# Optimization experiments

Measured on AMD Instinct MI355X. Metric: run time of the kernel, lower is better.

Reference implementation:

```python
import jax, jax.numpy as jnp
import numpy as np

T, N, E, D = 4, 50000, 800000, 256
VOCAB = 64000


def _gcn_layer(x, row, col, w, W, b, n):
    # PyG GCNConv: add self-loops (weight 1), symmetric normalization on
    # weighted in-degree (target/col), h = x @ W, scatter-add, then + bias.
    loops = jnp.arange(n, dtype=row.dtype)
    row2 = jnp.concatenate([row, loops])
    col2 = jnp.concatenate([col, loops])
    w2 = jnp.concatenate([w, jnp.ones((n,), x.dtype)])
    deg = jax.ops.segment_sum(w2, col2, num_segments=n)
    dinv = jnp.where(deg > 0, jax.lax.rsqrt(deg), 0.0)
    norm = dinv[row2] * w2 * dinv[col2]              # [E+N]
    h = x @ W                                        # [N, D]
    out = jax.ops.segment_sum(norm[:, None] * h[row2], col2, num_segments=n)
    return out + b


def _encode_timestep(ids, row, col, w, emb, W1, b1, W2, b2, W3, b3):
    x = emb[ids]                                     # [N, D] embedding lookup
    x = _gcn_layer(x, row, col, w, W1, b1, ids.shape[0])
    x = _gcn_layer(x, row, col, w, W2, b2, ids.shape[0])
    x = _gcn_layer(x, row, col, w, W3, b3, ids.shape[0])
    return x


def setup_inputs() -> dict:
    key = jax.random.key(0)
    ks = jax.random.split(key, 8)
    scale = 1.0 / np.sqrt(D)
    return {
        "node_features": jax.random.randint(ks[0], (T, N), 0, VOCAB, dtype=jnp.int32),
        "edge_index": jax.random.randint(ks[1], (T, 2, E), 0, N, dtype=jnp.int32),
        "edge_weight": jax.random.uniform(ks[2], (T, E), dtype=jnp.float32),
        "emb": jax.random.normal(ks[3], (VOCAB, D), dtype=jnp.float32),
        "W1": jax.random.normal(ks[4], (D, D), dtype=jnp.float32) * scale,
        "b1": jnp.zeros((D,), jnp.float32),
        "W2": jax.random.normal(ks[5], (D, D), dtype=jnp.float32) * scale,
        "b2": jnp.zeros((D,), jnp.float32),
        "W3": jax.random.normal(ks[6], (D, D), dtype=jnp.float32) * scale,
        "b3": jnp.zeros((D,), jnp.float32),
    }


def reference(node_features, edge_index, edge_weight, emb, W1, b1, W2, b2, W3, b3):
    outs = []
    for t in range(node_features.shape[0]):  # fixed small timestep count
        outs.append(_encode_timestep(node_features[t], edge_index[t, 0],
                                     edge_index[t, 1], edge_weight[t],
                                     emb, W1, b1, W2, b2, W3, b3))
    return jnp.concatenate(outs, axis=0)  # [T*N, D]
```

## Files before the change

kernel.cpp:

```cpp
#include <hip/hip_runtime.h>

#define T_STEPS 4
#define NN 50000
#define EE 800000
#define DD 256
#define VOCAB 64000
#define NB ((NN + 255) / 256)

typedef __attribute__((ext_vector_type(8))) short short8;
typedef __attribute__((ext_vector_type(4))) float floatx4;

__device__ __forceinline__ unsigned short f2bf(float f) {
    unsigned u = __float_as_uint(f);
    return (unsigned short)((u + 0x7FFFu + ((u >> 16) & 1u)) >> 16);
}
__device__ __forceinline__ float bf2f(unsigned short s) {
    return __uint_as_float(((unsigned)s) << 16);
}

__device__ __forceinline__ void async16(const unsigned short* g, unsigned short* l) {
    __builtin_amdgcn_global_load_lds(
        (const __attribute__((address_space(1))) void*)g,
        (__attribute__((address_space(3))) void*)l, 16, 0, 0);
}

__global__ __launch_bounds__(256) void init_deg_cnt(float* __restrict__ deg,
                                                    int* __restrict__ cnt, int n) {
    int i = blockIdx.x * 256 + threadIdx.x;
    if (i < n) { deg[i] = 1.0f; cnt[i] = 0; }
}

__global__ __launch_bounds__(256) void edge_deg_cnt(const int* __restrict__ col,
                                                    const float* __restrict__ w,
                                                    float* __restrict__ deg,
                                                    int* __restrict__ cnt, int e) {
    int i = blockIdx.x * 256 + threadIdx.x;
    if (i < e) {
        int c = col[i];
        atomicAdd(&deg[c], w[i]);
        atomicAdd(&cnt[c], 1);
    }
}

__global__ __launch_bounds__(256) void dinv_bsums(const float* __restrict__ deg,
                                                  float* __restrict__ dinv,
                                                  float* __restrict__ s1,
                                                  const int* __restrict__ cnt,
                                                  int* __restrict__ bsum, int n) {
    int i = blockIdx.x * 256 + threadIdx.x;
    if (i < n) {
        float d = deg[i];
        float r = d > 0.0f ? rsqrtf(d) : 0.0f;
        dinv[i] = r;
        s1[i] = r * r;
    }
    __shared__ int sm[256];
    sm[threadIdx.x] = (i < n) ? cnt[i] : 0;
    __syncthreads();
    for (int s = 128; s > 0; s >>= 1) {
        if ((int)threadIdx.x < s) sm[threadIdx.x] += sm[threadIdx.x + s];
        __syncthreads();
    }
    if (threadIdx.x == 0) bsum[blockIdx.x] = sm[0];
}

__global__ __launch_bounds__(256) void scan_bsum(const int* __restrict__ bsum,
                                                 int* __restrict__ boff, int nb) {
    __shared__ int sm[256];
    int v = ((int)threadIdx.x < nb) ? bsum[threadIdx.x] : 0;
    sm[threadIdx.x] = v;
    __syncthreads();
    for (int o = 1; o < 256; o <<= 1) {
        int t = (threadIdx.x >= (unsigned)o) ? sm[threadIdx.x - o] : 0;
        __syncthreads();
        sm[threadIdx.x] += t;
        __syncthreads();
    }
    if ((int)threadIdx.x < nb) boff[threadIdx.x] = sm[threadIdx.x] - v;
}

__global__ __launch_bounds__(256) void scan_final(const int* __restrict__ cnt,
                                                  const int* __restrict__ boff,
                                                  int* __restrict__ colptr,
                                                  int* __restrict__ next, int n, int e) {
    __shared__ int sm[256];
    int i = blockIdx.x * 256 + threadIdx.x;
    int v = (i < n) ? cnt[i] : 0;
    sm[threadIdx.x] = v;
    __syncthreads();
    for (int o = 1; o < 256; o <<= 1) {
        int t = (threadIdx.x >= (unsigned)o) ? sm[threadIdx.x - o] : 0;
        __syncthreads();
        sm[threadIdx.x] += t;
        __syncthreads();
    }
    int excl = sm[threadIdx.x] - v + boff[blockIdx.x];
    if (i < n) { colptr[i] = excl; next[i] = excl; }
    if (i == 0) colptr[n] = e;
}

__global__ __launch_bounds__(256) void fill_csr(const int* __restrict__ row,
                                                const int* __restrict__ col,
                                                const float* __restrict__ w,
                                                const float* __restrict__ dinv,
                                                int* __restrict__ next,
                                                int2* __restrict__ edges,
                                                float* __restrict__ s1, int e) {
    int i = blockIdx.x * 256 + threadIdx.x;
    if (i < e) {
        int r = row[i], c = col[i];
        float nm = dinv[r] * w[i] * dinv[c];
        int p = atomicAdd(&next[c], 1);
        edges[p] = make_int2(r, __float_as_int(nm));
        atomicAdd(&s1[c], nm);
    }
}

__global__ __launch_bounds__(256) void matmul256(const float* __restrict__ A,
                                                 const float* __restrict__ B,
                                                 float* __restrict__ C) {
    __shared__ float arow[256];
    int i = blockIdx.x, j = threadIdx.x;
    arow[j] = A[i * 256 + j];
    __syncthreads();
    float acc = 0.f;
#pragma unroll 8
    for (int k = 0; k < 256; ++k) acc += arow[k] * B[k * 256 + j];
    C[i * 256 + j] = acc;
}

__global__ __launch_bounds__(256) void matvec256(const float* __restrict__ x,
                                                 const float* __restrict__ W,
                                                 float* __restrict__ y) {
    __shared__ float xs[256];
    int j = threadIdx.x;
    xs[j] = x[j];
    __syncthreads();
    float acc = 0.f;
#pragma unroll 8
    for (int k = 0; k < 256; ++k) acc += xs[k] * W[k * 256 + j];
    y[j] = acc;
}

__global__ __launch_bounds__(256) void convert_wc(const float* __restrict__ Wc,
                                                  unsigned short* __restrict__ wt) {
    int n = blockIdx.x;
    int k = threadIdx.x;
    wt[n * 256 + k] = f2bf(Wc[k * 256 + n]);
}

__global__ __launch_bounds__(256) void convert_emb(const float* __restrict__ emb,
                                                   unsigned short* __restrict__ ebf,
                                                   int total4) {
    int t = blockIdx.x * 256 + threadIdx.x;
    if (t < total4) {
        float4 v = ((const float4*)emb)[t];
        ushort4 o;
        o.x = f2bf(v.x); o.y = f2bf(v.y); o.z = f2bf(v.z); o.w = f2bf(v.w);
        ((ushort4*)ebf)[t] = o;
    }
}

__global__ __launch_bounds__(256) void mfma_gemm(const int* __restrict__ ids,
                                                 const unsigned short* __restrict__ ebf,
                                                 const unsigned short* __restrict__ wt,
                                                 unsigned short* __restrict__ h2,
                                                 int M) {
    __shared__ __align__(16) unsigned short As[128 * 32];
    __shared__ __align__(16) unsigned short Bs[256 * 32];

    int tid = threadIdx.x;
    int lane = tid & 63;
    int wave = tid >> 6;
    int row0 = blockIdx.x * 128;
    int wm = (wave & 1) * 64;
    int wn = (wave >> 1) * 128;
    int quad = lane >> 4;
    int cl = lane & 15;

    int uA0 = tid, uA1 = 256 + tid;
    int cA0 = uA0 >> 7, mA0 = uA0 & 127;
    int cA1 = uA1 >> 7;
    int gr = row0 + mA0; if (gr >= M) gr = M - 1;
    int id0 = ids[gr];
    const unsigned short* srcA0 = ebf + (size_t)id0 * 256 + cA0 * 8;
    const unsigned short* srcA1 = ebf + (size_t)id0 * 256 + cA1 * 8;
    unsigned short* dstA0 = As + uA0 * 8;
    unsigned short* dstA1 = As + uA1 * 8;

    const unsigned short* srcB = wt + (size_t)tid * 256;
    unsigned short* dstBbase = Bs + tid * 8;

    floatx4 acc[4][8] = {};

    for (int k0 = 0; k0 < 256; k0 += 32) {
        if (k0) __syncthreads();
        async16(srcA0 + k0, dstA0);
        async16(srcA1 + k0, dstA1);
#pragma unroll
        for (int s5 = 0; s5 < 4; ++s5)
            async16(srcB + s5 * 8 + k0, dstBbase + s5 * 2048);
        __syncthreads();

        short8 af[4], bfr[8];
#pragma unroll
        for (int i = 0; i < 4; ++i)
            af[i] = *(const short8*)&As[(quad * 128 + wm + i * 16 + cl) * 8];
#pragma unroll
        for (int j = 0; j < 8; ++j)
            bfr[j] = *(const short8*)&Bs[(quad * 256 + wn + j * 16 + cl) * 8];
#pragma unroll
        for (int i = 0; i < 4; ++i)
#pragma unroll
            for (int j = 0; j < 8; ++j)
                acc[i][j] = __builtin_amdgcn_mfma_f32_16x16x32_bf16(
                    af[i], bfr[j], acc[i][j], 0, 0, 0);
    }

#pragma unroll
    for (int i = 0; i < 4; ++i) {
#pragma unroll
        for (int r = 0; r < 4; ++r) {
            int gr2 = row0 + wm + i * 16 + quad * 4 + r;
            if (gr2 < M) {
                size_t base = (size_t)gr2 * 256 + wn + cl;
#pragma unroll
                for (int j = 0; j < 8; ++j)
                    h2[base + j * 16] = f2bf(acc[i][j][r]);
            }
        }
    }
}

__global__ __launch_bounds__(256) void agg_kernel(const unsigned short* __restrict__ h2,
                                                  const int* __restrict__ colptr,
                                                  const int2* __restrict__ edges,
                                                  const float* __restrict__ dinv,
                                                  const float* __restrict__ s1,
                                                  float* __restrict__ s2_out,
                                                  const float* __restrict__ s2,
                                                  const float* __restrict__ v1,
                                                  const float* __restrict__ v2,
                                                  const float* __restrict__ b3,
                                                  float* __restrict__ dstf,
                                                  unsigned short* __restrict__ dstb,
                                                  int n) {
    int wave = threadIdx.x >> 6;
    int lane = threadIdx.x & 63;
    int h = lane >> 5;
    int s = lane & 31;
    int c = blockIdx.x * 4 + wave;
    if (c >= n) return;
    int p0 = colptr[c];
    int p1 = colptr[c + 1];
    float di = dinv[c];
    float self = di * di;
    bool do_s2 = (s2_out != nullptr);

    float accA[8] = {}, accB[8] = {};
    float ssA = 0.f, ssB = 0.f;

    if (h == 0) {
        short8 v = *(const short8*)(h2 + (size_t)c * 256 + s * 8);
#pragma unroll
        for (int k = 0; k < 8; ++k) accA[k] += self * bf2f((unsigned short)v[k]);
    }

    int j = p0 + h;
    for (; j + 2 < p1; j += 4) {
        int2 e0 = edges[j];
        int2 e1 = edges[j + 2];
        float w0 = __int_as_float(e0.y);
        float w1 = __int_as_float(e1.y);
        short8 va = *(const short8*)(h2 + (size_t)e0.x * 256 + s * 8);
        short8 vb = *(const short8*)(h2 + (size_t)e1.x * 256 + s * 8);
        if (do_s2) { ssA += w0 * s1[e0.x]; ssB += w1 * s1[e1.x]; }
#pragma unroll
        for (int k = 0; k < 8; ++k) {
            accA[k] += w0 * bf2f((unsigned short)va[k]);
            accB[k] += w1 * bf2f((unsigned short)vb[k]);
        }
    }
    if (j < p1) {
        int2 e0 = edges[j];
        float w0 = __int_as_float(e0.y);
        short8 va = *(const short8*)(h2 + (size_t)e0.x * 256 + s * 8);
        if (do_s2) ssA += w0 * s1[e0.x];
#pragma unroll
        for (int k = 0; k < 8; ++k) accA[k] += w0 * bf2f((unsigned short)va[k]);
    }

    float tot[8];
#pragma unroll
    for (int k = 0; k < 8; ++k) {
        float o = accA[k] + accB[k];
        tot[k] = o + __shfl(o, lane ^ 32, 64);
    }
    if (do_s2) {
        float ss = ssA + ssB;
        ss += __shfl(ss, lane ^ 32, 64);
        if (lane == 0) s2_out[c] = self * s1[c] + ss;
    }

    if (dstb) {
        if (h == 0) {
            short8 o;
#pragma unroll
            for (int k = 0; k < 8; ++k) o[k] = (short)f2bf(tot[k]);
            *(short8*)(dstb + (size_t)c * 256 + s * 8) = o;
        }
    } else {
        if (h == 0) {
            float s1c = s1[c], s2c = s2[c];
            int f0 = s * 8;
            float ob[8];
#pragma unroll
            for (int k = 0; k < 8; ++k)
                ob[k] = tot[k] + s2c * v1[f0 + k] + s1c * v2[f0 + k] + b3[f0 + k];
            float* o = dstf + (size_t)c * 256 + f0;
            ((float4*)o)[0] = make_float4(ob[0], ob[1], ob[2], ob[3]);
            ((float4*)o)[1] = make_float4(ob[4], ob[5], ob[6], ob[7]);
        }
    }
}

extern "C" void kernel_launch(void* const* d_in, const int* in_sizes, int n_in,
                              void* d_out, int out_size, void* d_ws, size_t ws_size,
                              hipStream_t stream) {
    const int*   node_features = (const int*)d_in[0];
    const int*   edge_index    = (const int*)d_in[1];
    const float* edge_weight   = (const float*)d_in[2];
    const float* emb           = (const float*)d_in[3];
    const float* W1 = (const float*)d_in[4];
    const float* b1 = (const float*)d_in[5];
    const float* W2 = (const float*)d_in[6];
    const float* b2 = (const float*)d_in[7];
    const float* W3 = (const float*)d_in[8];
    const float* b3 = (const float*)d_in[9];
    float* out = (float*)d_out;

    char* ws = (char*)d_ws;
    size_t off = 0;
    auto alloc = [&](size_t bytes) -> void* {
        void* p = ws + off;
        off = (off + bytes + 255) & ~(size_t)255;
        return p;
    };
    unsigned short* ebf    = (unsigned short*)alloc((size_t)VOCAB * DD * 2);
    unsigned short* xb     = (unsigned short*)alloc((size_t)NN * DD * 2);
    unsigned short* h2     = (unsigned short*)alloc((size_t)NN * DD * 2);
    unsigned short* wtc    = (unsigned short*)alloc((size_t)DD * DD * 2);
    float* Wtmp   = (float*)alloc((size_t)DD * DD * 4);
    float* Wc32   = (float*)alloc((size_t)DD * DD * 4);
    float* u      = (float*)alloc((size_t)DD * 4);
    float* v1     = (float*)alloc((size_t)DD * 4);
    float* v2     = (float*)alloc((size_t)DD * 4);
    float* deg    = (float*)alloc((size_t)NN * 4);
    float* dinv   = (float*)alloc((size_t)NN * 4);
    float* s1v    = (float*)alloc((size_t)NN * 4);
    float* s2v    = (float*)alloc((size_t)NN * 4);
    int*   cnt    = (int*)alloc((size_t)NN * 4);
    int*   colptr = (int*)alloc((size_t)(NN + 1) * 4);
    int*   next   = (int*)alloc((size_t)NN * 4);
    int2*  edges  = (int2*)alloc((size_t)EE * 8);
    int*   bsum   = (int*)alloc((size_t)NB * 4);
    int*   boff   = (int*)alloc((size_t)NB * 4);
    (void)ws_size; (void)n_in; (void)in_sizes; (void)out_size;

    const int gN   = (NN + 255) / 256;
    const int gE   = (EE + 255) / 256;
    const int gAgg = (NN + 3) / 4;
    const int gEmb = (VOCAB * 64 + 255) / 256;
    const int gGemm = (NN + 127) / 128;

    convert_emb<<<gEmb, 256, 0, stream>>>(emb, ebf, VOCAB * 64);
    matmul256<<<256, 256, 0, stream>>>(W1, W2, Wtmp);
    matmul256<<<256, 256, 0, stream>>>(Wtmp, W3, Wc32);
    convert_wc<<<256, 256, 0, stream>>>(Wc32, wtc);
    matvec256<<<1, 256, 0, stream>>>(b1, W2, u);
    matvec256<<<1, 256, 0, stream>>>(u, W3, v1);
    matvec256<<<1, 256, 0, stream>>>(b2, W3, v2);

    for (int t = 0; t < T_STEPS; ++t) {
        const int*   ids = node_features + (size_t)t * NN;
        const int*   row = edge_index + (size_t)t * 2 * EE;
        const int*   col = row + EE;
        const float* w   = edge_weight + (size_t)t * EE;

        init_deg_cnt<<<gN, 256, 0, stream>>>(deg, cnt, NN);
        edge_deg_cnt<<<gE, 256, 0, stream>>>(col, w, deg, cnt, EE);
        dinv_bsums<<<gN, 256, 0, stream>>>(deg, dinv, s1v, cnt, bsum, NN);
        scan_bsum<<<1, 256, 0, stream>>>(bsum, boff, NB);
        scan_final<<<gN, 256, 0, stream>>>(cnt, boff, colptr, next, NN, EE);
        fill_csr<<<gE, 256, 0, stream>>>(row, col, w, dinv, next, edges, s1v, EE);

        mfma_gemm<<<gGemm, 256, 0, stream>>>(ids, ebf, wtc, h2, NN);

        agg_kernel<<<gAgg, 256, 0, stream>>>(h2, colptr, edges, dinv,
                                             s1v, s2v, nullptr, nullptr, nullptr, nullptr,
                                             nullptr, xb, NN);
        agg_kernel<<<gAgg, 256, 0, stream>>>(xb, colptr, edges, dinv,
                                             nullptr, nullptr, nullptr, nullptr, nullptr, nullptr,
                                             nullptr, h2, NN);
        agg_kernel<<<gAgg, 256, 0, stream>>>(h2, colptr, edges, dinv,
                                             s1v, nullptr, s2v, v1, v2, b3,
                                             out + (size_t)t * NN * DD, nullptr, NN);
    }
}
```

Before: 1.797 ms.

## Slice feature table into 32-column planes for cache-resident aggregation

The GEMM now writes the bf16 feature table as 8 column slices, each a contiguous [N,32] plane (about 3.2 MB per slice). The aggregation kernel launches one grid per slice, and each wave processes 16 edges at a time with 4 lanes per 64-byte row. The goal is to keep each slice's gather working set in L2/MALL so random neighbor gathers hit cache instead of HBM. In exchange, the edge list and colptr are read 8 times, the butterfly reduction across 16 edge groups costs extra shuffles, and reuse only happens if blocks of the same slice run at the same time.

```diff
diff --git a/kernel.cpp b/kernel.cpp
--- a/kernel.cpp
+++ b/kernel.cpp
@@ -6,6 +6,8 @@
 #define DD 256
 #define VOCAB 64000
 #define NB ((NN + 255) / 256)
+#define SLICES 8
+#define NBLK_C ((NN + 3) / 4)
 
 typedef __attribute__((ext_vector_type(8))) short short8;
 typedef __attribute__((ext_vector_type(4))) float floatx4;
@@ -223,16 +225,18 @@
         for (int r = 0; r < 4; ++r) {
             int gr2 = row0 + wm + i * 16 + quad * 4 + r;
             if (gr2 < M) {
-                size_t base = (size_t)gr2 * 256 + wn + cl;
-#pragma unroll
-                for (int j = 0; j < 8; ++j)
-                    h2[base + j * 16] = f2bf(acc[i][j][r]);
+#pragma unroll
+                for (int j = 0; j < 8; ++j) {
+                    int colf = wn + j * 16 + cl;
+                    int slice = colf >> 5, off = colf & 31;
+                    h2[((size_t)slice * M + gr2) * 32 + off] = f2bf(acc[i][j][r]);
+                }
             }
         }
     }
 }
 
-__global__ __launch_bounds__(256) void agg_kernel(const unsigned short* __restrict__ h2,
+__global__ __launch_bounds__(256) void agg_sliced(const unsigned short* __restrict__ tbl,
                                                   const int* __restrict__ colptr,
                                                   const int2* __restrict__ edges,
                                                   const float* __restrict__ dinv,
@@ -245,78 +249,63 @@
                                                   float* __restrict__ dstf,
                                                   unsigned short* __restrict__ dstb,
                                                   int n) {
+    int slice = blockIdx.x / NBLK_C;
+    int cblk  = blockIdx.x % NBLK_C;
     int wave = threadIdx.x >> 6;
     int lane = threadIdx.x & 63;
-    int h = lane >> 5;
-    int s = lane & 31;
-    int c = blockIdx.x * 4 + wave;
+    int e  = lane >> 2;
+    int f4 = lane & 3;
+    int c = cblk * 4 + wave;
     if (c >= n) return;
     int p0 = colptr[c];
     int p1 = colptr[c + 1];
     float di = dinv[c];
     float self = di * di;
-    bool do_s2 = (s2_out != nullptr);
-
-    float accA[8] = {}, accB[8] = {};
-    float ssA = 0.f, ssB = 0.f;
-
-    if (h == 0) {
-        short8 v = *(const short8*)(h2 + (size_t)c * 256 + s * 8);
-#pragma unroll
-        for (int k = 0; k < 8; ++k) accA[k] += self * bf2f((unsigned short)v[k]);
-    }
-
-    int j = p0 + h;
-    for (; j + 2 < p1; j += 4) {
-        int2 e0 = edges[j];
-        int2 e1 = edges[j + 2];
-        float w0 = __int_as_float(e0.y);
-        float w1 = __int_as_float(e1.y);
-        short8 va = *(const short8*)(h2 + (size_t)e0.x * 256 + s * 8);
-        short8 vb = *(const short8*)(h2 + (size_t)e1.x * 256 + s * 8);
-        if (do_s2) { ssA += w0 * s1[e0.x]; ssB += w1 * s1[e1.x]; }
-#pragma unroll
-        for (int k = 0; k < 8; ++k) {
-            accA[k] += w0 * bf2f((unsigned short)va[k]);
-            accB[k] += w1 * bf2f((unsigned short)vb[k]);
+    bool do_s2 = (s2_out != nullptr) && (slice == 0);
+
+    const unsigned short* tb = tbl + (size_t)slice * n * 32;
+    float acc[8] = {};
+    float ss = 0.f;
+
+    if (e == 0) {
+        short8 v = *(const short8*)(tb + (size_t)c * 32 + f4 * 8);
+#pragma unroll
+        for (int k = 0; k < 8; ++k) acc[k] += self * bf2f((unsigned short)v[k]);
+    }
+
+    for (int j0 = p0; j0 < p1; j0 += 16) {
+        int jj = j0 + e;
+        if (jj < p1) {
+            int2 ed = edges[jj];
+            float w = __int_as_float(ed.y);
+            short8 v = *(const short8*)(tb + (size_t)ed.x * 32 + f4 * 8);
+            if (do_s2 && f4 == 0) ss += w * s1[ed.x];
+#pragma unroll
+            for (int k = 0; k < 8; ++k) acc[k] += w * bf2f((unsigned short)v[k]);
         }
     }
-    if (j < p1) {
-        int2 e0 = edges[j];
-        float w0 = __int_as_float(e0.y);
-        short8 va = *(const short8*)(h2 + (size_t)e0.x * 256 + s * 8);
-        if (do_s2) ssA += w0 * s1[e0.x];
-#pragma unroll
-        for (int k = 0; k < 8; ++k) accA[k] += w0 * bf2f((unsigned short)va[k]);
-    }
-
-    float tot[8];
-#pragma unroll
-    for (int k = 0; k < 8; ++k) {
-        float o = accA[k] + accB[k];
-        tot[k] = o + __shfl(o, lane ^ 32, 64);
-    }
-    if (do_s2) {
-        float ss = ssA + ssB;
-        ss += __shfl(ss, lane ^ 32, 64);
-        if (lane == 0) s2_out[c] = self * s1[c] + ss;
-    }
-
-    if (dstb) {
-        if (h == 0) {
+
+#pragma unroll
+    for (int m = 4; m <= 32; m <<= 1) {
+#pragma unroll
+        for (int k = 0; k < 8; ++k) acc[k] += __shfl_xor(acc[k], m, 64);
+        if (do_s2) ss += __shfl_xor(ss, m, 64);
+    }
+    if (do_s2 && lane == 0) s2_out[c] = self * s1[c] + ss;
+
+    if (e == 0) {
+        if (dstb) {
             short8 o;
 #pragma unroll
-            for (int k = 0; k < 8; ++k) o[k] = (short)f2bf(tot[k]);
-            *(short8*)(dstb + (size_t)c * 256 + s * 8) = o;
-        }
-    } else {
-        if (h == 0) {
+            for (int k = 0; k < 8; ++k) o[k] = (short)f2bf(acc[k]);
+            *(short8*)(dstb + ((size_t)slice * n + c) * 32 + f4 * 8) = o;
+        } else {
+            int f0 = slice * 32 + f4 * 8;
             float s1c = s1[c], s2c = s2[c];
-            int f0 = s * 8;
             float ob[8];
 #pragma unroll
             for (int k = 0; k < 8; ++k)
-                ob[k] = tot[k] + s2c * v1[f0 + k] + s1c * v2[f0 + k] + b3[f0 + k];
+                ob[k] = acc[k] + s2c * v1[f0 + k] + s1c * v2[f0 + k] + b3[f0 + k];
             float* o = dstf + (size_t)c * 256 + f0;
             ((float4*)o)[0] = make_float4(ob[0], ob[1], ob[2], ob[3]);
             ((float4*)o)[1] = make_float4(ob[4], ob[5], ob[6], ob[7]);
@@ -367,10 +356,10 @@
     int*   boff   = (int*)alloc((size_t)NB * 4);
     (void)ws_size; (void)n_in; (void)in_sizes; (void)out_size;
 
-    const int gN   = (NN + 255) / 256;
-    const int gE   = (EE + 255) / 256;
-    const int gAgg = (NN + 3) / 4;
-    const int gEmb = (VOCAB * 64 + 255) / 256;
+    const int gN    = (NN + 255) / 256;
+    const int gE    = (EE + 255) / 256;
+    const int gAgg  = SLICES * NBLK_C;
+    const int gEmb  = (VOCAB * 64 + 255) / 256;
     const int gGemm = (NN + 127) / 128;
 
     convert_emb<<<gEmb, 256, 0, stream>>>(emb, ebf, VOCAB * 64);
@@ -396,13 +385,13 @@
 
         mfma_gemm<<<gGemm, 256, 0, stream>>>(ids, ebf, wtc, h2, NN);
 
-        agg_kernel<<<gAgg, 256, 0, stream>>>(h2, colptr, edges, dinv,
+        agg_sliced<<<gAgg, 256, 0, stream>>>(h2, colptr, edges, dinv,
                                              s1v, s2v, nullptr, nullptr, nullptr, nullptr,
                                              nullptr, xb, NN);
-        agg_kernel<<<gAgg, 256, 0, stream>>>(xb, colptr, edges, dinv,
+        agg_sliced<<<gAgg, 256, 0, stream>>>(xb, colptr, edges, dinv,
                                              nullptr, nullptr, nullptr, nullptr, nullptr, nullptr,
                                              nullptr, h2, NN);
-        agg_kernel<<<gAgg, 256, 0, stream>>>(h2, colptr, edges, dinv,
+        agg_sliced<<<gAgg, 256, 0, stream>>>(h2, colptr, edges, dinv,
                                              s1v, nullptr, s2v, v1, v2, b3,
                                              out + (size_t)t * NN * DD, nullptr, NN);
     }
```

Result: slower. 2.976 ms (+65.7%).
